# Kernel tuning notes

Hardware: AMD Instinct MI355X
Metric: run time of the kernel (lower is better)

## Reference

```python
import jax, jax.numpy as jnp
import numpy as np

N_NODES = 100000
N_EDGES = 1600000
IN_CH, HID_CH, OUT_CH = 64, 64, 16
N_REL = 8


def setup_inputs() -> dict:
    key = jax.random.key(0)
    ks = jax.random.split(key, 10)
    x = jax.random.normal(ks[0], (N_NODES, IN_CH), dtype=jnp.float32)
    edge_index = jax.random.randint(ks[1], (2, N_EDGES), 0, N_NODES, dtype=jnp.int64)
    edge_type = jax.random.randint(ks[2], (N_EDGES,), 0, N_REL, dtype=jnp.int64)
    # RGCNConv params: per-relation weight, root weight, bias (Glorot-ish scale)
    def glorot(k, shape):
        fan = shape[-2] + shape[-1]
        return jax.random.normal(k, shape, dtype=jnp.float32) * jnp.sqrt(2.0 / fan)
    W1 = glorot(ks[3], (N_REL, IN_CH, HID_CH))
    root1 = glorot(ks[4], (IN_CH, HID_CH))
    b1 = jnp.zeros((HID_CH,), dtype=jnp.float32)
    W2 = glorot(ks[5], (N_REL, HID_CH, OUT_CH))
    root2 = glorot(ks[6], (HID_CH, OUT_CH))
    b2 = jnp.zeros((OUT_CH,), dtype=jnp.float32)
    return {"x": x, "edge_index": edge_index, "edge_type": edge_type,
            "W1": W1, "root1": root1, "b1": b1,
            "W2": W2, "root2": root2, "b2": b2}


def rgcn_conv(x, src, dst, edge_type, W_rel, W_root, bias):
    """PyG RGCNConv: out_i = x_i @ W_root + b + sum_r mean_{j in N_r(i)} x_j @ W_r.
    Mean is linear, so aggregate raw features per relation, then transform."""
    n = x.shape[0]
    xs = x[src]  # [E, F] gathered source features (hot memory-bound op)
    out = x @ W_root + bias
    for r in range(W_rel.shape[0]):  # small fixed relation count
        mask = (edge_type == r).astype(x.dtype)  # [E]
        agg = jax.ops.segment_sum(xs * mask[:, None], dst, num_segments=n)  # [N, F]
        cnt = jax.ops.segment_sum(mask, dst, num_segments=n)  # [N]
        agg = agg / jnp.clip(cnt, 1.0)[:, None]  # mean aggr; 0 when no edges
        out = out + agg @ W_rel[r]
    return out


def reference(x, edge_index, edge_type, W1, root1, b1, W2, root2, b2):
    src, dst = edge_index[0], edge_index[1]
    h = rgcn_conv(x, src, dst, edge_type, W1, root1, b1)
    h = jax.nn.relu(h)
    h = rgcn_conv(h, src, dst, edge_type, W2, root2, b2)
    # global_mean_pool with a single graph: mean over nodes -> [1, out]
    g = jnp.mean(h, axis=0, keepdims=True)
    return jax.nn.log_softmax(g, axis=1)
```

## Files before the change

### kernel.cpp

```cpp
#include <hip/hip_runtime.h>
#include <hip/hip_bf16.h>


#define CH 64
#define BK_EDGES 2048
#define CAP 12288
#define KB 128

typedef __attribute__((ext_vector_type(8))) short short8;
typedef __attribute__((ext_vector_type(4))) float f32x4;
typedef __attribute__((ext_vector_type(2))) float f32x2;

__device__ inline ushort f2bf(float f) {
    unsigned b = __float_as_uint(f);
    unsigned r = (b + 0x7FFFu + ((b >> 16) & 1u)) >> 16;
    return (ushort)r;
}
__device__ inline float bf2f(ushort u) {
    return __uint_as_float(((unsigned)u) << 16);
}

__device__ inline void acc8fp8(float* a, uint2 w, float m) {
    f32x2 p;
    p = __builtin_amdgcn_cvt_pk_f32_fp8(w.x, 0); a[0] += m * p.x; a[1] += m * p.y;
    p = __builtin_amdgcn_cvt_pk_f32_fp8(w.x, 1); a[2] += m * p.x; a[3] += m * p.y;
    p = __builtin_amdgcn_cvt_pk_f32_fp8(w.y, 0); a[4] += m * p.x; a[5] += m * p.y;
    p = __builtin_amdgcn_cvt_pk_f32_fp8(w.y, 1); a[6] += m * p.x; a[7] += m * p.y;
}


__global__ __launch_bounds__(256) void prep_kernel(
    const int* __restrict__ src, const int* __restrict__ dst,
    const int* __restrict__ etype, const float* __restrict__ x,
    const float* __restrict__ W1, const float* __restrict__ root1,
    int* __restrict__ gBucketCnt, int2* __restrict__ bucket_buf,
    ushort* __restrict__ xbf, unsigned char* __restrict__ xq,
    ushort* __restrict__ wf,
    int E, int N, int nBin, int nXbf)
{
    __shared__ int s_k[BK_EDGES];
    __shared__ int s_y[BK_EDGES];
    __shared__ int hist[256], scanv[256], lcur[256], bstart[256], gbase[256];
    const int t = threadIdx.x;
    const int bid = blockIdx.x;

    if (bid >= nBin) {
        if (bid < nBin + nXbf) {
            int i = (bid - nBin) * 256 + t;
            if (i < N * CH / 4) {
                float4 v = ((const float4*)x)[i];
                ((ushort4*)xbf)[i] = make_ushort4(f2bf(v.x), f2bf(v.y), f2bf(v.z), f2bf(v.w));
                int p8 = __builtin_amdgcn_cvt_pk_fp8_f32(v.x, v.y, 0, 0);
                p8 = __builtin_amdgcn_cvt_pk_fp8_f32(v.z, v.w, p8, 1);
                ((unsigned int*)xq)[i] = (unsigned int)p8;
            }
        } else {
            int idx = (bid - nBin - nXbf) * 256 + t;
            if (idx < 9 * 2 * 4 * 64 * 8) {
                int j    = idx & 7;
                int lane = (idx >> 3) & 63;
                int ct   = (idx >> 9) & 3;
                int ks   = (idx >> 11) & 1;
                int rel  = idx >> 12;
                int k = ks * 32 + (lane >> 4) * 8 + j;
                int n = ct * 16 + (lane & 15);
                float v = (rel < 8) ? W1[((size_t)rel * 64 + k) * 64 + n]
                                    : root1[(size_t)k * 64 + n];
                wf[idx] = f2bf(v);
            }
        }
        return;
    }

    const int e0 = bid * BK_EDGES;
    const int cnt = min(BK_EDGES, E - e0);

    hist[t] = 0;
    __syncthreads();

    int myb[8], myk[8], myy[8];
    #pragma unroll
    for (int i = 0; i < 8; ++i) {
        int li = t + i * 256;
        if (li < cnt) {
            int e = e0 + li;
            int r = etype[e];
            int k = r * N + dst[e];
            myk[i] = k;
            myy[i] = (r << 17) | src[e];
            myb[i] = k >> 12;
            atomicAdd(&hist[myb[i]], 1);
        } else myb[i] = -1;
    }
    __syncthreads();

    int v = hist[t];
    scanv[t] = v;
    __syncthreads();
    for (int off = 1; off < 256; off <<= 1) {
        int u = (t >= off) ? scanv[t - off] : 0;
        __syncthreads();
        scanv[t] += u;
        __syncthreads();
    }
    int excl = scanv[t] - v;
    bstart[t] = excl;
    lcur[t] = excl;
    __syncthreads();

    #pragma unroll
    for (int i = 0; i < 8; ++i) {
        if (myb[i] >= 0) {
            int p = atomicAdd(&lcur[myb[i]], 1);
            s_k[p] = myk[i];
            s_y[p] = myy[i];
        }
    }
    __syncthreads();

    if (v > 0) gbase[t] = atomicAdd(&gBucketCnt[t], v);
    __syncthreads();

    for (int p = t; p < cnt; p += 256) {
        int k = s_k[p];
        int b = k >> 12;
        int gp = gbase[b] + (p - bstart[b]);
        if (gp < CAP)
            bucket_buf[(size_t)b * CAP + gp] = make_int2(k, s_y[p]);
    }
}


__global__ __launch_bounds__(1024) void build_kernel(
    const int2* __restrict__ bucket_buf, const int* __restrict__ gBucketCnt,
    int* __restrict__ rowptr, float* __restrict__ inv,
    int* __restrict__ perm, int N)
{
    __shared__ int hist[4096];
    __shared__ int cur[4096];
    __shared__ int part[1024];
    const int b = blockIdx.x;
    const int t = threadIdx.x;
    const int nb = min(gBucketCnt[b], CAP);
    const int2* rec = bucket_buf + (size_t)b * CAP;

    int bc = (t < 256) ? gBucketCnt[t] : 0;
    part[t] = bc;
    __syncthreads();
    for (int off = 1; off < 1024; off <<= 1) {
        int u = (t >= off) ? part[t - off] : 0;
        __syncthreads();
        part[t] += u;
        __syncthreads();
    }
    __shared__ int baseS;
    if (t == b) baseS = part[t] - bc;
    __syncthreads();
    const int base = baseS;

    for (int i = t; i < 4096; i += 1024) hist[i] = 0;
    __syncthreads();
    for (int j = t; j < nb; j += 1024) atomicAdd(&hist[rec[j].x & 4095], 1);
    __syncthreads();

    const int i0 = t * 4;
    int h0 = hist[i0], h1 = hist[i0 + 1], h2 = hist[i0 + 2], h3 = hist[i0 + 3];
    int s = h0 + h1 + h2 + h3;
    part[t] = s;
    __syncthreads();
    for (int off = 1; off < 1024; off <<= 1) {
        int u = (t >= off) ? part[t - off] : 0;
        __syncthreads();
        part[t] += u;
        __syncthreads();
    }
    int run = base + part[t] - s;
    int hk[4] = {h0, h1, h2, h3};
    #pragma unroll
    for (int k = 0; k < 4; ++k) {
        cur[i0 + k] = run;
        rowptr[b * 4096 + i0 + k] = run;
        inv[b * 4096 + i0 + k] = 1.0f / (float)max(hk[k], 1);
        run += hk[k];
    }
    __syncthreads();

    for (int j = t; j < nb; j += 1024) {
        int k = rec[j].x, y = rec[j].y;
        int lk = k & 4095;
        int pos = atomicAdd(&cur[lk], 1);
        perm[pos] = y & 0x1FFFF;
    }
}


__global__ __launch_bounds__(256) void rgcn1_fused_kernel(
    const int* __restrict__ rowptr, const int* __restrict__ perm,
    const float* __restrict__ inv, const ushort* __restrict__ xbf,
    const unsigned char* __restrict__ xq,
    const ushort* __restrict__ wfrag, const float* __restrict__ b1,
    const int* __restrict__ srcE, const int* __restrict__ dstE,
    const int* __restrict__ etypeE, float* __restrict__ kappa,
    float* __restrict__ h, int N, int E)
{
    if (blockIdx.x < KB) {
        const int chunk = (E + KB - 1) / KB;
        const int lo = blockIdx.x * chunk;
        const int hi = min(lo + chunk, E);
        for (int e = lo + (int)threadIdx.x; e < hi; e += 256) {
            int r = etypeE[e];
            int d = dstE[e];
            int s = srcE[e];
            unsafeAtomicAdd(&kappa[(s << 3) | r], inv[(size_t)r * N + d]);
        }
        return;
    }

    __shared__ ushort Abuf[4][16 * 72];
    __shared__ int    rpS[4][144];
    __shared__ float  invS[4][128];
    const int widx = threadIdx.x >> 6;
    const int lane = threadIdx.x & 63;
    const int wid = ((blockIdx.x - KB) << 2) | widx;
    const int base = wid << 4;
    if (base >= N) return;

    const int m0 = lane & 15;
    const int q  = lane >> 4;
    const int sg = lane >> 3;
    const int cg = lane & 7;
    ushort* ab = Abuf[widx];
    int*    rpL = rpS[widx];
    float*  ivL = invS[widx];

    for (int i = lane; i < 136; i += 64) {
        int r = i / 17, mm = i - r * 17;
        rpL[i] = rowptr[(size_t)r * N + base + mm];
    }
    for (int i = lane; i < 128; i += 64)
        ivL[i] = inv[(size_t)(i >> 4) * N + base + (i & 15)];

    f32x4 acc4[4];
    #pragma unroll
    for (int ct = 0; ct < 4; ++ct) acc4[ct] = (f32x4)(0.0f);

    for (int r = 0; r < 8; ++r) {
        const int iA = r * 17 + sg;
        const int iB = iA + 8;
        int jA = rpL[iA], eA = rpL[iA + 1];
        int jB = rpL[iB], eB = rpL[iB + 1];
        float a[8] = {}, bacc[8] = {};
        int s0A = perm[(jA     < eA) ? jA     : 0];
        int s1A = perm[(jA + 1 < eA) ? jA + 1 : 0];
        int s0B = perm[(jB     < eB) ? jB     : 0];
        int s1B = perm[(jB + 1 < eB) ? jB + 1 : 0];
        while (jA < eA || jB < eB) {
            uint2 w0A = *(const uint2*)(xq + (size_t)s0A * CH + (cg << 3));
            uint2 w1A = *(const uint2*)(xq + (size_t)s1A * CH + (cg << 3));
            uint2 w0B = *(const uint2*)(xq + (size_t)s0B * CH + (cg << 3));
            uint2 w1B = *(const uint2*)(xq + (size_t)s1B * CH + (cg << 3));
            int t0A = perm[(jA + 2 < eA) ? jA + 2 : 0];
            int t1A = perm[(jA + 3 < eA) ? jA + 3 : 0];
            int t0B = perm[(jB + 2 < eB) ? jB + 2 : 0];
            int t1B = perm[(jB + 3 < eB) ? jB + 3 : 0];
            float m0A = (jA     < eA) ? 1.f : 0.f;
            float m1A = (jA + 1 < eA) ? 1.f : 0.f;
            float m0B = (jB     < eB) ? 1.f : 0.f;
            float m1B = (jB + 1 < eB) ? 1.f : 0.f;
            acc8fp8(a,    w0A, m0A);
            acc8fp8(a,    w1A, m1A);
            acc8fp8(bacc, w0B, m0B);
            acc8fp8(bacc, w1B, m1B);
            s0A = t0A; s1A = t1A; s0B = t0B; s1B = t1B;
            jA += 2; jB += 2;
        }
        const float ivA = ivL[(r << 4) | sg];
        const float ivB = ivL[(r << 4) | (8 + sg)];
        short8 oA, oB;
        #pragma unroll
        for (int k = 0; k < 8; ++k) {
            oA[k] = (short)f2bf(a[k] * ivA);
            oB[k] = (short)f2bf(bacc[k] * ivB);
        }
        *(short8*)&ab[sg * 72 + (cg << 3)]       = oA;
        *(short8*)&ab[(8 + sg) * 72 + (cg << 3)] = oB;

        #pragma unroll
        for (int s = 0; s < 2; ++s) {
            short8 av = *(short8*)&ab[m0 * 72 + s * 32 + q * 8];
            #pragma unroll
            for (int ct = 0; ct < 4; ++ct) {
                short8 bv = *(const short8*)&wfrag[(((size_t)(r * 2 + s) * 4 + ct) * 64 + lane) * 8];
                acc4[ct] = __builtin_amdgcn_mfma_f32_16x16x32_bf16(av, bv, acc4[ct], 0, 0, 0);
            }
        }
    }

    {
        int node = min(base + m0, N - 1);
        #pragma unroll
        for (int s = 0; s < 2; ++s) {
            short8 av = *(const short8*)&xbf[(size_t)node * CH + s * 32 + q * 8];
            #pragma unroll
            for (int ct = 0; ct < 4; ++ct) {
                short8 bv = *(const short8*)&wfrag[(((size_t)(8 * 2 + s) * 4 + ct) * 64 + lane) * 8];
                acc4[ct] = __builtin_amdgcn_mfma_f32_16x16x32_bf16(av, bv, acc4[ct], 0, 0, 0);
            }
        }
    }

    #pragma unroll
    for (int ct = 0; ct < 4; ++ct) {
        int c = ct * 16 + m0;
        float bb = b1[c];
        #pragma unroll
        for (int v = 0; v < 4; ++v) {
            int node = base + q * 4 + v;
            if (node < N)
                h[(size_t)node * CH + c] = fmaxf(acc4[ct][v] + bb, 0.f);
        }
    }
}


__global__ __launch_bounds__(256) void kred_kernel(
    const float* __restrict__ h, const float* __restrict__ kappa,
    float* __restrict__ sacc, int N)
{
    const int lane = threadIdx.x & 63;
    const int w = threadIdx.x >> 6;
    int wave = (blockIdx.x << 2) | w;
    const int wstride = gridDim.x << 2;
    float racc[9] = {};
    for (int i = wave; i < N; i += wstride) {
        float hv = h[(size_t)i * CH + lane];
        #pragma unroll
        for (int r = 0; r < 8; ++r) racc[r] += hv * kappa[i * 8 + r];
        racc[8] += hv;
    }
    __shared__ float red[4][9][64];
    #pragma unroll
    for (int r = 0; r < 9; ++r) red[w][r][lane] = racc[r];
    __syncthreads();
    if (w == 0) {
        #pragma unroll
        for (int r = 0; r < 9; ++r) {
            float s4 = red[0][r][lane] + red[1][r][lane] + red[2][r][lane] + red[3][r][lane];
            unsafeAtomicAdd(&sacc[r * 64 + lane], s4);
        }
    }
}

__global__ void finalize_kernel(const float* __restrict__ sacc, const float* __restrict__ root2,
                                const float* __restrict__ W2, const float* __restrict__ b2,
                                float* __restrict__ out, float invN)
{
    __shared__ float g[16];
    int t = threadIdx.x;
    if (t < 16) {
        const float* s0 = sacc + 512;
        float acc = 0.f;
        for (int c = 0; c < 64; ++c) acc += s0[c] * root2[c * 16 + t];
        for (int r = 0; r < 8; ++r) {
            const float* sr = sacc + r * 64;
            for (int c = 0; c < 64; ++c) acc += sr[c] * W2[(r * 64 + c) * 16 + t];
        }
        g[t] = acc * invN + b2[t];
    }
    __syncthreads();
    if (t < 16) {
        float m = -1e30f;
        for (int i = 0; i < 16; ++i) m = fmaxf(m, g[i]);
        float s = 0.f;
        for (int i = 0; i < 16; ++i) s += expf(g[i] - m);
        out[t] = g[t] - (m + logf(s));
    }
}


extern "C" void kernel_launch(void* const* d_in, const int* in_sizes, int n_in,
                              void* d_out, int out_size, void* d_ws, size_t ws_size,
                              hipStream_t stream)
{
    const float* x     = (const float*)d_in[0];
    const int*   eidx  = (const int*)d_in[1];
    const int*   etype = (const int*)d_in[2];
    const float* W1    = (const float*)d_in[3];
    const float* root1 = (const float*)d_in[4];
    const float* b1    = (const float*)d_in[5];
    const float* W2    = (const float*)d_in[6];
    const float* root2 = (const float*)d_in[7];
    const float* b2    = (const float*)d_in[8];
    float* out = (float*)d_out;

    const int E = in_sizes[1] / 2;
    const int N = in_sizes[0] / CH;
    const int NKEY = N * 8;
    const int NBUK = (NKEY + 4095) / 4096;
    const int KSPACE = NBUK << 12;
    const int* srcI = eidx;
    const int* dstI = eidx + E;

    int* wsi = (int*)d_ws;
    int*   gBucketCnt = wsi;
    float* sacc       = (float*)(gBucketCnt + 256);
    float* kappa      = sacc + 576;
    float* inv        = kappa + NKEY;
    int*   rowptr     = (int*)(inv + KSPACE);
    int*   perm       = rowptr + KSPACE + 16;
    size_t off = (size_t)((perm + E) - wsi);
    off = (off + 1) & ~(size_t)1;
    int2*  bucket_buf = (int2*)(wsi + off);
    off += (size_t)NBUK * CAP * 2;
    off = (off + 7) & ~(size_t)7;
    ushort* xbf = (ushort*)(wsi + off);
    ushort* wfg = xbf + (size_t)N * CH;
    unsigned char* xq = (unsigned char*)(wfg + 36864);
    float*  h   = (float*)(xq + (size_t)N * CH);

    hipMemsetAsync(d_ws, 0, (size_t)(256 + 576 + NKEY) * 4, stream);

    const int nBin = (E + BK_EDGES - 1) / BK_EDGES;
    const int nXbf = (N * CH / 4 + 255) / 256;
    const int nWf  = (36864 + 255) / 256;
    prep_kernel<<<nBin + nXbf + nWf, 256, 0, stream>>>(
        srcI, dstI, etype, x, W1, root1, gBucketCnt, bucket_buf, xbf, xq, wfg,
        E, N, nBin, nXbf);

    build_kernel<<<NBUK, 1024, 0, stream>>>(
        bucket_buf, gBucketCnt, rowptr, inv, perm, N);

    const int tiles = (N + 15) / 16;
    rgcn1_fused_kernel<<<KB + (tiles + 3) / 4, 256, 0, stream>>>(
        rowptr, perm, inv, xbf, xq, wfg, b1, srcI, dstI, etype, kappa, h, N, E);

    kred_kernel<<<1024, 256, 0, stream>>>(h, kappa, sacc, N);
    finalize_kernel<<<1, 64, 0, stream>>>(sacc, root2, W2, b2, out, 1.0f / (float)N);
}
```

Baseline: 293.0 us.

## Fuse kappa accumulation into CSR build and store hidden layer in bf16

Computes the per-source, per-relation kappa weights inside build_kernel while edges are scattered into perm, using the local histogram count for 1/deg. This removes the separate edge pass in the fused layer-1 kernel, which re-read src, dst and type and gathered inv for every edge. The hidden activations h are also stored as bf16 instead of fp32, halving write and read traffic in kred. The bf16 h adds rounding error, and the kappa atomics now run inside build_kernel.

```diff
diff --git a/kernel.cpp b/kernel.cpp
--- a/kernel.cpp
+++ b/kernel.cpp
@@ -5,7 +5,6 @@
 #define CH 64
 #define BK_EDGES 2048
 #define CAP 12288
-#define KB 128
 
 typedef __attribute__((ext_vector_type(8))) short short8;
 typedef __attribute__((ext_vector_type(4))) float f32x4;
@@ -134,7 +133,7 @@
 __global__ __launch_bounds__(1024) void build_kernel(
     const int2* __restrict__ bucket_buf, const int* __restrict__ gBucketCnt,
     int* __restrict__ rowptr, float* __restrict__ inv,
-    int* __restrict__ perm, int N)
+    int* __restrict__ perm, float* __restrict__ kappa, int N)
 {
     __shared__ int hist[4096];
     __shared__ int cur[4096];
@@ -189,7 +188,10 @@
         int k = rec[j].x, y = rec[j].y;
         int lk = k & 4095;
         int pos = atomicAdd(&cur[lk], 1);
-        perm[pos] = y & 0x1FFFF;
+        int srcn = y & 0x1FFFF;
+        perm[pos] = srcn;
+        float iv = 1.0f / (float)hist[lk];
+        unsafeAtomicAdd(&kappa[(srcn << 3) | (y >> 17)], iv);
     }
 }
 
@@ -199,29 +201,14 @@
     const float* __restrict__ inv, const ushort* __restrict__ xbf,
     const unsigned char* __restrict__ xq,
     const ushort* __restrict__ wfrag, const float* __restrict__ b1,
-    const int* __restrict__ srcE, const int* __restrict__ dstE,
-    const int* __restrict__ etypeE, float* __restrict__ kappa,
-    float* __restrict__ h, int N, int E)
-{
-    if (blockIdx.x < KB) {
-        const int chunk = (E + KB - 1) / KB;
-        const int lo = blockIdx.x * chunk;
-        const int hi = min(lo + chunk, E);
-        for (int e = lo + (int)threadIdx.x; e < hi; e += 256) {
-            int r = etypeE[e];
-            int d = dstE[e];
-            int s = srcE[e];
-            unsafeAtomicAdd(&kappa[(s << 3) | r], inv[(size_t)r * N + d]);
-        }
-        return;
-    }
-
+    ushort* __restrict__ h, int N)
+{
     __shared__ ushort Abuf[4][16 * 72];
     __shared__ int    rpS[4][144];
     __shared__ float  invS[4][128];
     const int widx = threadIdx.x >> 6;
     const int lane = threadIdx.x & 63;
-    const int wid = ((blockIdx.x - KB) << 2) | widx;
+    const int wid = (blockIdx.x << 2) | widx;
     const int base = wid << 4;
     if (base >= N) return;
 
@@ -317,14 +304,14 @@
         for (int v = 0; v < 4; ++v) {
             int node = base + q * 4 + v;
             if (node < N)
-                h[(size_t)node * CH + c] = fmaxf(acc4[ct][v] + bb, 0.f);
+                h[(size_t)node * CH + c] = f2bf(fmaxf(acc4[ct][v] + bb, 0.f));
         }
     }
 }
 
 
 __global__ __launch_bounds__(256) void kred_kernel(
-    const float* __restrict__ h, const float* __restrict__ kappa,
+    const ushort* __restrict__ h, const float* __restrict__ kappa,
     float* __restrict__ sacc, int N)
 {
     const int lane = threadIdx.x & 63;
@@ -333,7 +320,7 @@
     const int wstride = gridDim.x << 2;
     float racc[9] = {};
     for (int i = wave; i < N; i += wstride) {
-        float hv = h[(size_t)i * CH + lane];
+        float hv = bf2f(h[(size_t)i * CH + lane]);
         #pragma unroll
         for (int r = 0; r < 8; ++r) racc[r] += hv * kappa[i * 8 + r];
         racc[8] += hv;
@@ -416,7 +403,7 @@
     ushort* xbf = (ushort*)(wsi + off);
     ushort* wfg = xbf + (size_t)N * CH;
     unsigned char* xq = (unsigned char*)(wfg + 36864);
-    float*  h   = (float*)(xq + (size_t)N * CH);
+    ushort* h = (ushort*)(xq + (size_t)N * CH);
 
     hipMemsetAsync(d_ws, 0, (size_t)(256 + 576 + NKEY) * 4, stream);
 
@@ -428,11 +415,11 @@
         E, N, nBin, nXbf);
 
     build_kernel<<<NBUK, 1024, 0, stream>>>(
-        bucket_buf, gBucketCnt, rowptr, inv, perm, N);
+        bucket_buf, gBucketCnt, rowptr, inv, perm, kappa, N);
 
     const int tiles = (N + 15) / 16;
-    rgcn1_fused_kernel<<<KB + (tiles + 3) / 4, 256, 0, stream>>>(
-        rowptr, perm, inv, xbf, xq, wfg, b1, srcI, dstI, etype, kappa, h, N, E);
+    rgcn1_fused_kernel<<<(tiles + 3) / 4, 256, 0, stream>>>(
+        rowptr, perm, inv, xbf, xq, wfg, b1, h, N);
 
     kred_kernel<<<1024, 256, 0, stream>>>(h, kappa, sacc, N);
     finalize_kernel<<<1, 64, 0, stream>>>(sacc, root2, W2, b2, out, 1.0f / (float)N);
```

New measurement: 336.5 us. +14.9%, slower.
